# Optimization experiments

Hardware: AMD Instinct MI355X
Metric: run time of the kernel (lower is better)

The kernel has to match this reference:

```python
import jax, jax.numpy as jnp
import numpy as np
from jax import lax

D_MODEL = 256
D_STATE = 16
BATCH = 4
SEQ = 16384
LN_EPS = 1e-5


def setup_inputs() -> dict:
    key = jax.random.key(0)
    ks = jax.random.split(key, 16)
    d, s = D_MODEL, D_STATE
    lim = 1.0 / np.sqrt(d)
    u = lambda k, shape, l: jax.random.uniform(k, shape, jnp.float32, -l, l)
    return {
        "x": jax.random.normal(ks[0], (BATCH, SEQ, d), jnp.float32),
        # forward branch params (torch Linear stored as (in, out))
        "W_fproj": u(ks[1], (d, 2 * d), lim),
        "b_fproj": u(ks[2], (2 * d,), lim),
        "A_f": jax.random.normal(ks[3], (s, d), jnp.float32),
        "W_fgate": u(ks[4], (d, s), lim),
        "b_fgate": u(ks[5], (s,), lim),
        # backward branch params
        "W_bproj": u(ks[6], (d, 2 * d), lim),
        "b_bproj": u(ks[7], (2 * d,), lim),
        "A_b": jax.random.normal(ks[8], (s, d), jnp.float32),
        "W_bgate": u(ks[9], (d, s), lim),
        "b_bgate": u(ks[10], (s,), lim),
        # output proj + layernorm
        "W_out": u(ks[11], (2 * d, d), 1.0 / np.sqrt(2 * d)),
        "b_out": u(ks[12], (d,), 1.0 / np.sqrt(2 * d)),
        "ln_g": jnp.ones((d,), jnp.float32),
        "ln_b": jnp.zeros((d,), jnp.float32),
    }


def _scan_dir(x, W_proj, b_proj, A, W_gate, b_gate):
    """One direction: gated state-space scan. x: (B,S,D) -> (B,S,D)."""
    B, S, D = x.shape
    proj = x @ W_proj + b_proj            # (B,S,2D)
    value = proj[..., D:]                 # the 'gate' chunk is unused in the original
    gw = jax.nn.sigmoid(value @ W_gate + b_gate)  # (B,S,d_state)

    def step(state, inp):
        g, v = inp                        # g:(B,Ns), v:(B,D)
        gi = g[:, :, None]                # (B,Ns,1)
        upd = A[None, :, :] * v[:, None, :]
        state = state * gi + upd * (1.0 - gi)
        out = (state * gi).sum(axis=1)    # (B,D)
        return state, out

    init = jnp.zeros((B, A.shape[0], D), x.dtype)
    _, outs = lax.scan(step, init, (gw.transpose(1, 0, 2), value.transpose(1, 0, 2)))
    return outs.transpose(1, 0, 2)        # (B,S,D)


def reference(x, W_fproj, b_fproj, A_f, W_fgate, b_fgate,
              W_bproj, b_bproj, A_b, W_bgate, b_bgate,
              W_out, b_out, ln_g, ln_b):
    fwd = _scan_dir(x, W_fproj, b_fproj, A_f, W_fgate, b_fgate)
    x_rev = jnp.flip(x, axis=1)
    bwd = jnp.flip(_scan_dir(x_rev, W_bproj, b_bproj, A_b, W_bgate, b_bgate), axis=1)
    combined = jnp.concatenate([fwd, bwd], axis=-1)    # (B,S,2D)
    out = combined @ W_out + b_out                     # (B,S,D)
    mu = out.mean(axis=-1, keepdims=True)
    var = out.var(axis=-1, keepdims=True)
    out = (out - mu) * lax.rsqrt(var + LN_EPS) * ln_g + ln_b
    return out  # dropout is identity in eval mode
```

## Files before the change

kernel.cpp:

```cpp
#include <hip/hip_runtime.h>

#define SEQ   16384
#define NB    4
#define NROWS 65536
#define NC    512
#define CL    32

typedef short bf16x8 __attribute__((ext_vector_type(8)));
typedef float f32x4  __attribute__((ext_vector_type(4)));
typedef float f32x2  __attribute__((ext_vector_type(2)));

__device__ inline float bf2f(ushort u) {
    unsigned int t = ((unsigned int)u) << 16;
    float f; __builtin_memcpy(&f, &t, 4); return f;
}
__device__ inline float bflo(uint u) {
    uint t = u << 16; float f; __builtin_memcpy(&f, &t, 4); return f;
}
__device__ inline float bfhi(uint u) {
    uint t = u & 0xffff0000u; float f; __builtin_memcpy(&f, &t, 4); return f;
}
__device__ inline ushort f2bf(float f) {
    unsigned int b; __builtin_memcpy(&b, &f, 4);
    unsigned int r = (b + 0x7FFFu + ((b >> 16) & 1u)) >> 16;
    return (ushort)r;
}

__device__ inline f32x2 pk_fma(f32x2 a, f32x2 b, f32x2 c) {
    f32x2 d;
    asm("v_pk_fma_f32 %0, %1, %2, %3" : "=v"(d) : "v"(a), "v"(b), "v"(c));
    return d;
}
__device__ inline f32x2 pk_mul(f32x2 a, f32x2 b) {
    f32x2 d;
    asm("v_pk_mul_f32 %0, %1, %2" : "=v"(d) : "v"(a), "v"(b));
    return d;
}
__device__ inline f32x2 pk_sub(f32x2 a, f32x2 b) {
    f32x2 d;
    asm("v_pk_add_f32 %0, %1, %2 neg_lo:[0,1] neg_hi:[0,1]" : "=v"(d) : "v"(a), "v"(b));
    return d;
}

__global__ __launch_bounds__(256) void prep_weights(
    const float* __restrict__ Wf, const float* __restrict__ Wb,
    const float* __restrict__ Wo, const float* __restrict__ Wgf,
    const float* __restrict__ Wgb, const float* __restrict__ bfp,
    const float* __restrict__ bbp, const float* __restrict__ A_f,
    const float* __restrict__ A_b,
    ushort* __restrict__ BTv, ushort* __restrict__ WoT,
    ushort* __restrict__ WgT, float* __restrict__ bias_v,
    float* __restrict__ AsT)
{
    int idx = blockIdx.x * 256 + threadIdx.x;
    if (idx < 131072) {
        int dir = idx >> 16, j = idx & 65535, n = j >> 8, k = j & 255;
        const float* W = dir ? Wb : Wf;
        BTv[idx] = f2bf(W[k * 512 + 256 + n]);
    } else if (idx < 262144) {
        int j = idx - 131072; int n = j >> 9, k = j & 511;
        WoT[j] = f2bf(Wo[k * 256 + n]);
    } else if (idx < 270336) {
        int j = idx - 262144; int dir = j >> 12, jj = j & 4095, s = jj >> 8, k = jj & 255;
        WgT[j] = f2bf((dir ? Wgb : Wgf)[k * 16 + s]);
    } else if (idx < 270848) {
        int j = idx - 270336; int dir = j >> 8, n = j & 255;
        bias_v[j] = (dir ? bbp : bfp)[256 + n];
    } else if (idx < 279040) {
        int j = idx - 270848; int dir = j >> 12, jj = j & 4095, d = jj >> 4, s = jj & 15;
        AsT[j] = (dir ? A_b : A_f)[s * 256 + d];
    }
}

__global__ __launch_bounds__(512) void gemm_value(
    const float* __restrict__ x, const ushort* __restrict__ BTv,
    const float* __restrict__ bias_v, ushort* __restrict__ value)
{
    __shared__ ushort Al[128 * 40];
    __shared__ ushort Bl[256 * 40];
    const int tid = threadIdx.x;
    const int m0 = blockIdx.y * 128, dir = blockIdx.x;
    const ushort* BT = BTv + dir * 65536;
    const int w = tid >> 6, l = tid & 63;
    const int wr = w >> 2, wc = w & 3;
    const int l15 = l & 15, lk = (l >> 4) * 8;
    f32x4 acc[4][4] = {};

    for (int kk = 0; kk < 256; kk += 32) {
        {
            int r = tid >> 2, c = (tid & 3) * 8;
            const float* xp = x + (size_t)(m0 + r) * 256 + kk + c;
            float4 a = *(const float4*)xp;
            float4 b = *(const float4*)(xp + 4);
            ushort u[8];
            u[0] = f2bf(a.x); u[1] = f2bf(a.y); u[2] = f2bf(a.z); u[3] = f2bf(a.w);
            u[4] = f2bf(b.x); u[5] = f2bf(b.y); u[6] = f2bf(b.z); u[7] = f2bf(b.w);
            *(uint4*)&Al[r * 40 + c] = *(uint4*)u;
        }
        #pragma unroll
        for (int i = 0; i < 2; ++i) {
            int idx = tid + i * 512; int r = idx >> 2, c = idx & 3;
            *(uint4*)&Bl[r * 40 + c * 8] = *(const uint4*)(BT + (size_t)r * 256 + kk + c * 8);
        }
        __syncthreads();
        bf16x8 af[4], bfr[4];
        #pragma unroll
        for (int m = 0; m < 4; ++m) af[m] = *(const bf16x8*)&Al[(wr * 64 + m * 16 + l15) * 40 + lk];
        #pragma unroll
        for (int n = 0; n < 4; ++n) bfr[n] = *(const bf16x8*)&Bl[(wc * 64 + n * 16 + l15) * 40 + lk];
        #pragma unroll
        for (int m = 0; m < 4; ++m)
            #pragma unroll
            for (int n = 0; n < 4; ++n)
                acc[m][n] = __builtin_amdgcn_mfma_f32_16x16x32_bf16(af[m], bfr[n], acc[m][n], 0, 0, 0);
        __syncthreads();
    }
    const int rbase = (l >> 4) * 4;
    #pragma unroll
    for (int m = 0; m < 4; ++m)
        #pragma unroll
        for (int n = 0; n < 4; ++n) {
            int col = wc * 64 + n * 16 + l15;
            float bv = bias_v[dir * 256 + col];
            #pragma unroll
            for (int r = 0; r < 4; ++r) {
                int row = m0 + wr * 64 + m * 16 + rbase + r;
                value[(size_t)row * 512 + dir * 256 + col] = f2bf(acc[m][n][r] + bv);
            }
        }
}

__global__ __launch_bounds__(256, 3) void gate_scan(
    const ushort* __restrict__ value, const ushort* __restrict__ WgT,
    const float* __restrict__ bgf, const float* __restrict__ bgb,
    float* __restrict__ gw, ushort* __restrict__ L16, float* __restrict__ P)
{
    __shared__ ushort Av[64 * 264];
    __shared__ float gsm[64 * 16];
    const int tid = threadIdx.x;
    const int r0 = blockIdx.x * 64, dir = blockIdx.y;
    #pragma unroll
    for (int i = 0; i < 8; ++i) {
        int idx = tid + i * 256; int r = idx >> 5, c = idx & 31;
        *(uint4*)&Av[r * 264 + c * 8] =
            *(const uint4*)(value + (size_t)(r0 + r) * 512 + dir * 256 + c * 8);
    }
    __syncthreads();
    const int w = tid >> 6, l = tid & 63, l15 = l & 15, lk = (l >> 4) * 8;
    const ushort* Wg = WgT + dir * 4096;
    f32x4 acc = {};
    #pragma unroll
    for (int kk = 0; kk < 256; kk += 32) {
        bf16x8 af = *(const bf16x8*)&Av[(w * 16 + l15) * 264 + kk + lk];
        bf16x8 bf = *(const bf16x8*)(Wg + l15 * 256 + kk + lk);
        acc = __builtin_amdgcn_mfma_f32_16x16x32_bf16(af, bf, acc, 0, 0, 0);
    }
    const float bgs = (dir ? bgb : bgf)[l15];
    const int rbase = (l >> 4) * 4;
    const int b = r0 >> 14, t0 = r0 & 16383;
    #pragma unroll
    for (int r = 0; r < 4; ++r) {
        int lr = w * 16 + rbase + r;
        float sv = 1.f / (1.f + __expf(-(acc[r] + bgs)));
        gsm[lr * 16 + l15] = sv;
        gw[((size_t)(dir * NB + b) * SEQ + t0 + lr) * 16 + l15] = sv;
    }
    __syncthreads();
    const int ci = tid >> 7, dp = tid & 127;
    const int chunk = (t0 >> 5) + ci;
    f32x2 c0[8] = {}, c1[8] = {};
    for (int i = 0; i < CL; ++i) {
        int row = dir ? (CL - 1 - i) : i;
        uint vv = *(const uint*)&Av[(ci * 32 + row) * 264 + dp * 2];
        float v0 = bflo(vv), v1 = bfhi(vv);
        f32x2 vd0 = {v0, v0}, vd1 = {v1, v1};
        #pragma unroll
        for (int sp = 0; sp < 8; ++sp) {
            f32x2 g = *(const f32x2*)&gsm[(ci * 32 + row) * 16 + sp * 2];
            c0[sp] = pk_fma(g, pk_sub(c0[sp], vd0), vd0);
            c1[sp] = pk_fma(g, pk_sub(c1[sp], vd1), vd1);
        }
    }
    {
        ushort ub[32];
        #pragma unroll
        for (int sp = 0; sp < 8; ++sp) {
            ub[2 * sp]      = f2bf(c0[sp].x);
            ub[2 * sp + 1]  = f2bf(c0[sp].y);
            ub[16 + 2 * sp]     = f2bf(c1[sp].x);
            ub[16 + 2 * sp + 1] = f2bf(c1[sp].y);
        }
        ushort* Lp = L16 + ((size_t)(dir * NB + b) * NC + chunk) * 4096 + dp * 32;
        #pragma unroll
        for (int q = 0; q < 4; ++q)
            *(uint4*)(Lp + q * 8) = *(uint4*)&ub[q * 8];
    }
    if (dp < 16) {
        float p = 1.f;
        for (int t = 0; t < CL; ++t) p *= gsm[(ci * 32 + t) * 16 + dp];
        P[((size_t)(dir * NB + b) * NC + chunk) * 16 + dp] = p;
    }
}

__global__ __launch_bounds__(256, 2) void chunk_scan(
    ushort* __restrict__ L16, const float* __restrict__ P)
{
    const int bid = blockIdx.x;
    const int dir = bid >> 6, b = (bid >> 4) & 3, dgrp = bid & 15;
    const int tid = threadIdx.x;
    const int s = tid & 15;
    const size_t cb = (size_t)(dir * NB + b) * NC;
    ushort* Lb = L16 + cb * 4096 + dgrp * 256 + tid;
    const float* Pb = P + cb * 16 + s;
    float e = 0.f;
    ushort lA[16], lB[16];
    float pA[16], pB[16];

#define LOADB(la, pa, ib) { _Pragma("unroll") \
    for (int j = 0; j < 16; ++j) { \
        int t = (ib) * 16 + j; int k = dir ? (NC - 1 - t) : t; \
        la[j] = Lb[(size_t)k * 4096]; pa[j] = Pb[k * 16]; } }
#define PROCB(la, pa, ib) { _Pragma("unroll") \
    for (int j = 0; j < 16; ++j) { \
        int t = (ib) * 16 + j; int k = dir ? (NC - 1 - t) : t; \
        Lb[(size_t)k * 4096] = f2bf(e); e = pa[j] * e + bf2f(la[j]); } }

    LOADB(lA, pA, 0)
    for (int ib = 0; ib < 32; ib += 2) {
        LOADB(lB, pB, ib + 1)
        PROCB(lA, pA, ib)
        if (ib + 2 < 32) { LOADB(lA, pA, ib + 2) }
        PROCB(lB, pB, ib + 1)
    }
#undef LOADB
#undef PROCB
}

__global__ __launch_bounds__(128, 4) void pass_c(
    ushort* __restrict__ value, const float* __restrict__ gw,
    const ushort* __restrict__ L16, const float* __restrict__ AsT)
{
    const int chunk = blockIdx.x, b = blockIdx.y, dir = blockIdx.z;
    const int tid = threadIdx.x;
    __shared__ float gs[CL * 16];
    const float* gwd = gw + ((size_t)(dir * NB + b) * SEQ + chunk * CL) * 16;
    ((float4*)gs)[tid] = ((const float4*)gwd)[tid];
    __syncthreads();
    ushort* vb = value + ((size_t)b * SEQ + chunk * CL) * 512 + dir * 256 + tid * 2;
    const float* Ad = AsT + dir * 4096 + tid * 32;
    const ushort* Lp = L16 + ((size_t)(dir * NB + b) * NC + chunk) * 4096 + tid * 32;
    f32x2 a0[8], a1[8], c0[8], c1[8];
    #pragma unroll
    for (int sp = 0; sp < 8; ++sp) {
        a0[sp] = *(const f32x2*)(Ad + sp * 2);
        a1[sp] = *(const f32x2*)(Ad + 16 + sp * 2);
        uint u0 = *(const uint*)(Lp + sp * 2);
        uint u1 = *(const uint*)(Lp + 16 + sp * 2);
        c0[sp].x = bflo(u0); c0[sp].y = bfhi(u0);
        c1[sp].x = bflo(u1); c1[sp].y = bfhi(u1);
    }
    uint vbuf[4];
    #pragma unroll
    for (int j = 0; j < 4; ++j) {
        int row = dir ? (CL - 1 - j) : j;
        vbuf[j] = *(const uint*)(vb + (size_t)row * 512);
    }
    for (int i0 = 0; i0 < CL; i0 += 4) {
        uint vcur[4];
        #pragma unroll
        for (int j = 0; j < 4; ++j) vcur[j] = vbuf[j];
        if (i0 + 4 < CL) {
            #pragma unroll
            for (int j = 0; j < 4; ++j) {
                int t = i0 + 4 + j;
                int row = dir ? (CL - 1 - t) : t;
                vbuf[j] = *(const uint*)(vb + (size_t)row * 512);
            }
        }
        #pragma unroll
        for (int j = 0; j < 4; ++j) {
            int t = i0 + j;
            int row = dir ? (CL - 1 - t) : t;
            float v0 = bflo(vcur[j]), v1 = bfhi(vcur[j]);
            f32x2 vd0 = {v0, v0}, vd1 = {v1, v1};
            f32x2 o0 = {0.f, 0.f}, o1 = {0.f, 0.f};
            #pragma unroll
            for (int sp = 0; sp < 8; ++sp) {
                f32x2 g = *(const f32x2*)&gs[row * 16 + sp * 2];
                c0[sp] = pk_fma(g, pk_sub(c0[sp], vd0), vd0);
                o0 = pk_fma(a0[sp], pk_mul(g, c0[sp]), o0);
                c1[sp] = pk_fma(g, pk_sub(c1[sp], vd1), vd1);
                o1 = pk_fma(a1[sp], pk_mul(g, c1[sp]), o1);
            }
            uint outv = (uint)f2bf(o0.x + o0.y) | ((uint)f2bf(o1.x + o1.y) << 16);
            *(uint*)(vb + (size_t)row * 512) = outv;
        }
    }
}

__global__ __launch_bounds__(512) void gemm_out_ln(
    const ushort* __restrict__ A, const ushort* __restrict__ BT,
    const float* __restrict__ b_out, const float* __restrict__ ln_g,
    const float* __restrict__ ln_b, float* __restrict__ out)
{
    __shared__ ushort Al[128 * 40];
    __shared__ ushort Bl[256 * 40];
    __shared__ float red[2][2][4][64];
    const int tid = threadIdx.x;
    const int m0 = blockIdx.x * 128;
    const int w = tid >> 6, l = tid & 63;
    const int wr = w >> 2, wc = w & 3;
    const int l15 = l & 15, lk = (l >> 4) * 8;
    f32x4 acc[4][4] = {};

    for (int kk = 0; kk < 512; kk += 32) {
        {
            int r = tid >> 2, c = tid & 3;
            *(uint4*)&Al[r * 40 + c * 8] = *(const uint4*)(A + (size_t)(m0 + r) * 512 + kk + c * 8);
        }
        #pragma unroll
        for (int i = 0; i < 2; ++i) {
            int idx = tid + i * 512; int r = idx >> 2, c = idx & 3;
            *(uint4*)&Bl[r * 40 + c * 8] = *(const uint4*)(BT + (size_t)r * 512 + kk + c * 8);
        }
        __syncthreads();
        bf16x8 af[4], bfr[4];
        #pragma unroll
        for (int m = 0; m < 4; ++m) af[m] = *(const bf16x8*)&Al[(wr * 64 + m * 16 + l15) * 40 + lk];
        #pragma unroll
        for (int n = 0; n < 4; ++n) bfr[n] = *(const bf16x8*)&Bl[(wc * 64 + n * 16 + l15) * 40 + lk];
        #pragma unroll
        for (int m = 0; m < 4; ++m)
            #pragma unroll
            for (int n = 0; n < 4; ++n)
                acc[m][n] = __builtin_amdgcn_mfma_f32_16x16x32_bf16(af[m], bfr[n], acc[m][n], 0, 0, 0);
        __syncthreads();
    }
    const int rbase = (l >> 4) * 4;
    float gg[4], bb[4];
    #pragma unroll
    for (int n = 0; n < 4; ++n) {
        int col = wc * 64 + n * 16 + l15;
        float bv = b_out[col];
        gg[n] = ln_g[col]; bb[n] = ln_b[col];
        #pragma unroll
        for (int m = 0; m < 4; ++m)
            #pragma unroll
            for (int r = 0; r < 4; ++r)
                acc[m][n][r] += bv;
    }
    float s1[4][4], s2[4][4];
    #pragma unroll
    for (int m = 0; m < 4; ++m)
        #pragma unroll
        for (int r = 0; r < 4; ++r) {
            float a_ = 0.f, b_ = 0.f;
            #pragma unroll
            for (int n = 0; n < 4; ++n) {
                float v = acc[m][n][r];
                a_ += v; b_ += v * v;
            }
            s1[m][r] = a_; s2[m][r] = b_;
        }
    #pragma unroll
    for (int mask = 1; mask < 16; mask <<= 1)
        #pragma unroll
        for (int m = 0; m < 4; ++m)
            #pragma unroll
            for (int r = 0; r < 4; ++r) {
                s1[m][r] += __shfl_xor(s1[m][r], mask, 64);
                s2[m][r] += __shfl_xor(s2[m][r], mask, 64);
            }
    if (l15 == 0) {
        #pragma unroll
        for (int m = 0; m < 4; ++m)
            #pragma unroll
            for (int r = 0; r < 4; ++r) {
                int row = m * 16 + rbase + r;
                red[0][wr][wc][row] = s1[m][r];
                red[1][wr][wc][row] = s2[m][r];
            }
    }
    __syncthreads();
    #pragma unroll
    for (int m = 0; m < 4; ++m)
        #pragma unroll
        for (int r = 0; r < 4; ++r) {
            int row = m * 16 + rbase + r;
            float t1 = red[0][wr][0][row] + red[0][wr][1][row] + red[0][wr][2][row] + red[0][wr][3][row];
            float t2 = red[1][wr][0][row] + red[1][wr][1][row] + red[1][wr][2][row] + red[1][wr][3][row];
            float mu = t1 * (1.f / 256.f);
            float var = t2 * (1.f / 256.f) - mu * mu;
            float rs = rsqrtf(var + 1e-5f);
            #pragma unroll
            for (int n = 0; n < 4; ++n) {
                int col = wc * 64 + n * 16 + l15;
                out[(size_t)(m0 + wr * 64 + row) * 256 + col] = (acc[m][n][r] - mu) * rs * gg[n] + bb[n];
            }
        }
}

extern "C" void kernel_launch(void* const* d_in, const int* in_sizes, int n_in,
                              void* d_out, int out_size, void* d_ws, size_t ws_size,
                              hipStream_t stream)
{
    const float* x       = (const float*)d_in[0];
    const float* W_fproj = (const float*)d_in[1];
    const float* b_fproj = (const float*)d_in[2];
    const float* A_f     = (const float*)d_in[3];
    const float* W_fgate = (const float*)d_in[4];
    const float* b_fgate = (const float*)d_in[5];
    const float* W_bproj = (const float*)d_in[6];
    const float* b_bproj = (const float*)d_in[7];
    const float* A_b     = (const float*)d_in[8];
    const float* W_bgate = (const float*)d_in[9];
    const float* b_bgate = (const float*)d_in[10];
    const float* W_out   = (const float*)d_in[11];
    const float* b_out   = (const float*)d_in[12];
    const float* ln_g    = (const float*)d_in[13];
    const float* ln_b    = (const float*)d_in[14];

    char* ws = (char*)d_ws;
    ushort* value  = (ushort*)(ws + 0);
    float*  gw     = (float*) (ws + 67108864);
    ushort* L16    = (ushort*)(ws + 75497472);
    float*  P      = (float*) (ws + 109051904);
    ushort* BTv    = (ushort*)(ws + 109314048);
    ushort* WoT    = (ushort*)(ws + 109576192);
    ushort* WgT    = (ushort*)(ws + 109838336);
    float*  bias_v = (float*) (ws + 109854720);
    float*  AsT    = (float*) (ws + 109856768);

    prep_weights<<<1090, 256, 0, stream>>>(W_fproj, W_bproj, W_out, W_fgate, W_bgate,
                                           b_fproj, b_bproj, A_f, A_b,
                                           BTv, WoT, WgT, bias_v, AsT);
    gemm_value<<<dim3(2, 512), 512, 0, stream>>>(x, BTv, bias_v, value);
    gate_scan<<<dim3(1024, 2), 256, 0, stream>>>(value, WgT, b_fgate, b_bgate, gw, L16, P);
    chunk_scan<<<128, 256, 0, stream>>>(L16, P);
    pass_c<<<dim3(NC, NB, 2), 128, 0, stream>>>(value, gw, L16, AsT);
    gemm_out_ln<<<512, 512, 0, stream>>>(value, WoT, b_out, ln_g, ln_b, (float*)d_out);
}
```

Before: 202.7 us.

## Map one thread per channel in chunk scans and stage pass_c values via LDS

gate_scan and pass_c now give each thread a single d channel instead of two channel pairs. In gate_scan a thread loops over both chunks; pass_c uses 256 threads per block. pass_c also stages the chunk's value tile in shared memory with coalesced 16-byte loads and stores, replacing strided 4-byte global accesses per row. This trades more threads and fewer registers per thread for extra LDS traffic and an added sync. gate_scan now does twice the serial work per thread.

```diff
diff --git a/kernel.cpp b/kernel.cpp
--- a/kernel.cpp
+++ b/kernel.cpp
@@ -130,7 +130,7 @@
         }
 }
 
-__global__ __launch_bounds__(256, 3) void gate_scan(
+__global__ __launch_bounds__(256) void gate_scan(
     const ushort* __restrict__ value, const ushort* __restrict__ WgT,
     const float* __restrict__ bgf, const float* __restrict__ bgb,
     float* __restrict__ gw, ushort* __restrict__ L16, float* __restrict__ P)
@@ -166,39 +166,36 @@
         gw[((size_t)(dir * NB + b) * SEQ + t0 + lr) * 16 + l15] = sv;
     }
     __syncthreads();
-    const int ci = tid >> 7, dp = tid & 127;
-    const int chunk = (t0 >> 5) + ci;
-    f32x2 c0[8] = {}, c1[8] = {};
-    for (int i = 0; i < CL; ++i) {
-        int row = dir ? (CL - 1 - i) : i;
-        uint vv = *(const uint*)&Av[(ci * 32 + row) * 264 + dp * 2];
-        float v0 = bflo(vv), v1 = bfhi(vv);
-        f32x2 vd0 = {v0, v0}, vd1 = {v1, v1};
+    const int d = tid;
+    #pragma unroll
+    for (int ci = 0; ci < 2; ++ci) {
+        const int chunk = (t0 >> 5) + ci;
+        f32x2 c[8] = {};
+        for (int i = 0; i < CL; ++i) {
+            int row = dir ? (CL - 1 - i) : i;
+            float v = bf2f(Av[(ci * 32 + row) * 264 + d]);
+            f32x2 vd = {v, v};
+            #pragma unroll
+            for (int sp = 0; sp < 8; ++sp) {
+                f32x2 g = *(const f32x2*)&gsm[(ci * 32 + row) * 16 + sp * 2];
+                c[sp] = pk_fma(g, pk_sub(c[sp], vd), vd);
+            }
+        }
+        ushort ub[16];
         #pragma unroll
         for (int sp = 0; sp < 8; ++sp) {
-            f32x2 g = *(const f32x2*)&gsm[(ci * 32 + row) * 16 + sp * 2];
-            c0[sp] = pk_fma(g, pk_sub(c0[sp], vd0), vd0);
-            c1[sp] = pk_fma(g, pk_sub(c1[sp], vd1), vd1);
-        }
-    }
-    {
-        ushort ub[32];
-        #pragma unroll
-        for (int sp = 0; sp < 8; ++sp) {
-            ub[2 * sp]      = f2bf(c0[sp].x);
-            ub[2 * sp + 1]  = f2bf(c0[sp].y);
-            ub[16 + 2 * sp]     = f2bf(c1[sp].x);
-            ub[16 + 2 * sp + 1] = f2bf(c1[sp].y);
-        }
-        ushort* Lp = L16 + ((size_t)(dir * NB + b) * NC + chunk) * 4096 + dp * 32;
-        #pragma unroll
-        for (int q = 0; q < 4; ++q)
-            *(uint4*)(Lp + q * 8) = *(uint4*)&ub[q * 8];
-    }
-    if (dp < 16) {
+            ub[2 * sp]     = f2bf(c[sp].x);
+            ub[2 * sp + 1] = f2bf(c[sp].y);
+        }
+        ushort* Lp = L16 + ((size_t)(dir * NB + b) * NC + chunk) * 4096 + d * 16;
+        *(uint4*)Lp       = *(uint4*)&ub[0];
+        *(uint4*)(Lp + 8) = *(uint4*)&ub[8];
+    }
+    if (tid < 32) {
+        int ci2 = tid >> 4, s = tid & 15;
         float p = 1.f;
-        for (int t = 0; t < CL; ++t) p *= gsm[(ci * 32 + t) * 16 + dp];
-        P[((size_t)(dir * NB + b) * NC + chunk) * 16 + dp] = p;
+        for (int t = 0; t < CL; ++t) p *= gsm[(ci2 * 32 + t) * 16 + s];
+        P[((size_t)(dir * NB + b) * NC + (t0 >> 5) + ci2) * 16 + s] = p;
     }
 }
 
@@ -236,65 +233,53 @@
 #undef PROCB
 }
 
-__global__ __launch_bounds__(128, 4) void pass_c(
+__global__ __launch_bounds__(256) void pass_c(
     ushort* __restrict__ value, const float* __restrict__ gw,
     const ushort* __restrict__ L16, const float* __restrict__ AsT)
 {
     const int chunk = blockIdx.x, b = blockIdx.y, dir = blockIdx.z;
     const int tid = threadIdx.x;
     __shared__ float gs[CL * 16];
+    __shared__ ushort vs[CL * 256];
     const float* gwd = gw + ((size_t)(dir * NB + b) * SEQ + chunk * CL) * 16;
-    ((float4*)gs)[tid] = ((const float4*)gwd)[tid];
+    if (tid < 128) ((float4*)gs)[tid] = ((const float4*)gwd)[tid];
+    ushort* vg = value + ((size_t)b * SEQ + chunk * CL) * 512 + dir * 256;
+    #pragma unroll
+    for (int i = 0; i < 4; ++i) {
+        int idx = tid + i * 256;
+        int r = idx >> 5, cc = idx & 31;
+        *(uint4*)&vs[r * 256 + cc * 8] = *(const uint4*)(vg + (size_t)r * 512 + cc * 8);
+    }
     __syncthreads();
-    ushort* vb = value + ((size_t)b * SEQ + chunk * CL) * 512 + dir * 256 + tid * 2;
-    const float* Ad = AsT + dir * 4096 + tid * 32;
-    const ushort* Lp = L16 + ((size_t)(dir * NB + b) * NC + chunk) * 4096 + tid * 32;
-    f32x2 a0[8], a1[8], c0[8], c1[8];
+    const int d = tid;
+    const float* Ad = AsT + dir * 4096 + d * 16;
+    const ushort* Lp = L16 + ((size_t)(dir * NB + b) * NC + chunk) * 4096 + d * 16;
+    f32x2 a[8], c[8];
     #pragma unroll
     for (int sp = 0; sp < 8; ++sp) {
-        a0[sp] = *(const f32x2*)(Ad + sp * 2);
-        a1[sp] = *(const f32x2*)(Ad + 16 + sp * 2);
-        uint u0 = *(const uint*)(Lp + sp * 2);
-        uint u1 = *(const uint*)(Lp + 16 + sp * 2);
-        c0[sp].x = bflo(u0); c0[sp].y = bfhi(u0);
-        c1[sp].x = bflo(u1); c1[sp].y = bfhi(u1);
-    }
-    uint vbuf[4];
-    #pragma unroll
-    for (int j = 0; j < 4; ++j) {
-        int row = dir ? (CL - 1 - j) : j;
-        vbuf[j] = *(const uint*)(vb + (size_t)row * 512);
-    }
-    for (int i0 = 0; i0 < CL; i0 += 4) {
-        uint vcur[4];
-        #pragma unroll
-        for (int j = 0; j < 4; ++j) vcur[j] = vbuf[j];
-        if (i0 + 4 < CL) {
-            #pragma unroll
-            for (int j = 0; j < 4; ++j) {
-                int t = i0 + 4 + j;
-                int row = dir ? (CL - 1 - t) : t;
-                vbuf[j] = *(const uint*)(vb + (size_t)row * 512);
-            }
-        }
-        #pragma unroll
-        for (int j = 0; j < 4; ++j) {
-            int t = i0 + j;
-            int row = dir ? (CL - 1 - t) : t;
-            float v0 = bflo(vcur[j]), v1 = bfhi(vcur[j]);
-            f32x2 vd0 = {v0, v0}, vd1 = {v1, v1};
-            f32x2 o0 = {0.f, 0.f}, o1 = {0.f, 0.f};
-            #pragma unroll
-            for (int sp = 0; sp < 8; ++sp) {
-                f32x2 g = *(const f32x2*)&gs[row * 16 + sp * 2];
-                c0[sp] = pk_fma(g, pk_sub(c0[sp], vd0), vd0);
-                o0 = pk_fma(a0[sp], pk_mul(g, c0[sp]), o0);
-                c1[sp] = pk_fma(g, pk_sub(c1[sp], vd1), vd1);
-                o1 = pk_fma(a1[sp], pk_mul(g, c1[sp]), o1);
-            }
-            uint outv = (uint)f2bf(o0.x + o0.y) | ((uint)f2bf(o1.x + o1.y) << 16);
-            *(uint*)(vb + (size_t)row * 512) = outv;
-        }
+        a[sp] = *(const f32x2*)(Ad + sp * 2);
+        uint u = *(const uint*)(Lp + sp * 2);
+        c[sp].x = bflo(u); c[sp].y = bfhi(u);
+    }
+    for (int i = 0; i < CL; ++i) {
+        int row = dir ? (CL - 1 - i) : i;
+        float v = bf2f(vs[row * 256 + d]);
+        f32x2 vd = {v, v};
+        f32x2 o = {0.f, 0.f};
+        #pragma unroll
+        for (int sp = 0; sp < 8; ++sp) {
+            f32x2 g = *(const f32x2*)&gs[row * 16 + sp * 2];
+            c[sp] = pk_fma(g, pk_sub(c[sp], vd), vd);
+            o = pk_fma(a[sp], pk_mul(g, c[sp]), o);
+        }
+        vs[row * 256 + d] = f2bf(o.x + o.y);
+    }
+    __syncthreads();
+    #pragma unroll
+    for (int i = 0; i < 4; ++i) {
+        int idx = tid + i * 256;
+        int r = idx >> 5, cc = idx & 31;
+        *(uint4*)(vg + (size_t)r * 512 + cc * 8) = *(uint4*)&vs[r * 256 + cc * 8];
     }
 }
 
@@ -437,6 +422,6 @@
     gemm_value<<<dim3(2, 512), 512, 0, stream>>>(x, BTv, bias_v, value);
     gate_scan<<<dim3(1024, 2), 256, 0, stream>>>(value, WgT, b_fgate, b_bgate, gw, L16, P);
     chunk_scan<<<128, 256, 0, stream>>>(L16, P);
-    pass_c<<<dim3(NC, NB, 2), 128, 0, stream>>>(value, gw, L16, AsT);
+    pass_c<<<dim3(NC, NB, 2), 256, 0, stream>>>(value, gw, L16, AsT);
     gemm_out_ln<<<512, 512, 0, stream>>>(value, WoT, b_out, ln_g, ln_b, (float*)d_out);
 }
```

New measurement: 210.4 us. 3.8% more time.
